# Performance work log

Hardware: AMD Instinct MI355X
Metric: run time of the kernel (lower is better)

Reference implementation:

```python
import jax, jax.numpy as jnp
import numpy as np

N = 20000          # nodes
F = 64             # num_features
H = 128            # hidden_channels
K = 6              # kNN neighbors (includes self, matching torch_cluster.knn(x, x, k))
E = 120000         # unused edge_index length


def knn_indices(x, k):
    # squared euclidean pairwise distances: [N, N]
    sq = jnp.sum(x * x, axis=-1)
    dist2 = sq[:, None] + sq[None, :] - 2.0 * (x @ x.T)
    # k smallest distances per row (self included, dist ~0)
    _, idx = jax.lax.top_k(-dist2, k)   # [N, K]
    return idx


def setup_inputs() -> dict:
    key = jax.random.key(0)
    ks = jax.random.split(key, 6)
    x = jax.random.normal(ks[0], (N, F), dtype=jnp.float32)
    edge_index = jax.random.randint(ks[1], (2, E), 0, N, dtype=jnp.int64)
    W1 = jax.random.normal(ks[2], (2 * F, H), dtype=jnp.float32) * 0.05
    b1 = jnp.zeros((H,), dtype=jnp.float32)
    W2 = jax.random.normal(ks[3], (H, H), dtype=jnp.float32) * 0.05
    b2 = jnp.zeros((H,), dtype=jnp.float32)
    return {"x": x, "edge_index": edge_index, "W1": W1, "b1": b1, "W2": W2, "b2": b2}


def reference(x, edge_index, W1, b1, W2, b2):
    # DynamicEdgeConv: recompute kNN graph each forward (edge_index arg unused, as in source)
    idx = knn_indices(x, K)                       # [N, K] neighbor indices j for each center i
    xi = jnp.broadcast_to(x[:, None, :], (N, K, F))  # center features
    xj = x[idx]                                   # neighbor features  [N, K, F]
    msg = jnp.concatenate([xi, xj - xi], axis=-1)    # [N, K, 2F]
    h = jax.nn.relu(jnp.einsum('nkf,fh->nkh', msg, W1) + b1)
    h = jnp.einsum('nkh,hg->nkg', h, W2) + b2     # [N, K, H]
    return jnp.max(h, axis=1)                     # max aggregation -> [N, H]
```

## Files before the change

kernel.cpp:

```cpp
#include <hip/hip_runtime.h>


#define N_NODES 20000
#define FDIM 64
#define KNN 6
#define HID 128
#define N_PAD 20480
#define NTILES 625
#define PREP_TILES 628
#define NBLK 157
#define NCHUNK 3
#define TPC 209
#define RPB 256
#define TILE_J 64
#define MAX_CHUNKS 10

typedef __attribute__((ext_vector_type(8))) short short8;
typedef __attribute__((ext_vector_type(16))) float f32x16;

#define MFMAB(A, B, C) __builtin_amdgcn_mfma_f32_32x32x16_bf16((A), (B), (C), 0, 0, 0)
#define ROFF(r) (((r) & 3) + 8 * ((r) >> 2))

#define INSERT_CAND(bd, bj, dv, jv) do {                                      \
  if ((dv) < bd[5]) {                                                         \
    const bool c0 = (dv) < bd[0], c1 = (dv) < bd[1], c2 = (dv) < bd[2];       \
    const bool c3 = (dv) < bd[3], c4 = (dv) < bd[4];                          \
    bd[5] = c4 ? bd[4] : (dv);              bj[5] = c4 ? bj[4] : (jv);        \
    bd[4] = c4 ? (c3 ? bd[3] : (dv)) : bd[4]; bj[4] = c4 ? (c3 ? bj[3] : (jv)) : bj[4]; \
    bd[3] = c3 ? (c2 ? bd[2] : (dv)) : bd[3]; bj[3] = c3 ? (c2 ? bj[2] : (jv)) : bj[3]; \
    bd[2] = c2 ? (c1 ? bd[1] : (dv)) : bd[2]; bj[2] = c2 ? (c1 ? bj[1] : (jv)) : bj[2]; \
    bd[1] = c1 ? (c0 ? bd[0] : (dv)) : bd[1]; bj[1] = c1 ? (c0 ? bj[0] : (jv)) : bj[1]; \
    bd[0] = c0 ? (dv) : bd[0];              bj[0] = c0 ? (jv) : bj[0];        \
  }                                                                           \
} while (0)

#define LEXLT(dv, jv, ds, js) (((dv) < (ds)) || ((dv) == (ds) && (jv) < (js)))
#define INSERT_TIE(bd, bj, dv, jv) do {                                       \
  if (LEXLT((dv), (jv), bd[5], bj[5])) {                                      \
    const bool c0 = LEXLT((dv), (jv), bd[0], bj[0]);                          \
    const bool c1 = LEXLT((dv), (jv), bd[1], bj[1]);                          \
    const bool c2 = LEXLT((dv), (jv), bd[2], bj[2]);                          \
    const bool c3 = LEXLT((dv), (jv), bd[3], bj[3]);                          \
    const bool c4 = LEXLT((dv), (jv), bd[4], bj[4]);                          \
    bd[5] = c4 ? bd[4] : (dv);              bj[5] = c4 ? bj[4] : (jv);        \
    bd[4] = c4 ? (c3 ? bd[3] : (dv)) : bd[4]; bj[4] = c4 ? (c3 ? bj[3] : (jv)) : bj[4]; \
    bd[3] = c3 ? (c2 ? bd[2] : (dv)) : bd[3]; bj[3] = c3 ? (c2 ? bj[2] : (jv)) : bj[3]; \
    bd[2] = c2 ? (c1 ? bd[1] : (dv)) : bd[2]; bj[2] = c2 ? (c1 ? bj[1] : (jv)) : bj[2]; \
    bd[1] = c1 ? (c0 ? bd[0] : (dv)) : bd[1]; bj[1] = c1 ? (c0 ? bj[0] : (jv)) : bj[1]; \
    bd[0] = c0 ? (dv) : bd[0];              bj[0] = c0 ? (jv) : bj[0];        \
  }                                                                           \
} while (0)

__device__ __forceinline__ f32x16 zero16() {
  f32x16 v;
#pragma unroll
  for (int i = 0; i < 16; ++i) v[i] = 0.f;
  return v;
}

__device__ __forceinline__ unsigned short bf16_rne(float x) {
  unsigned u = __float_as_uint(x);
  u += 0x7fffu + ((u >> 16) & 1u);
  return (unsigned short)(u >> 16);
}
__device__ __forceinline__ float bf16_tof(unsigned short h) {
  return __uint_as_float(((unsigned)h) << 16);
}

__global__ void prep_kernel(const float* __restrict__ x, short* __restrict__ xa,
                            short* __restrict__ xb, short* __restrict__ xc,
                            float* __restrict__ sq) {
  const int n = blockIdx.x * blockDim.x + threadIdx.x;
  if (n >= PREP_TILES * 32) return;
  const int tile = n >> 5, row = n & 31;
  unsigned short a[FDIM], b[FDIM], c[FDIM];
  float s = 0.f;
  if (n < N_NODES) {
    const float4* r4 = (const float4*)(x + (size_t)n * FDIM);
#pragma unroll
    for (int q = 0; q < 16; ++q) {
      const float4 v = r4[q];
      const float vv[4] = {v.x, v.y, v.z, v.w};
#pragma unroll
      for (int e = 0; e < 4; ++e) {
        const float xv = vv[e];
        s = fmaf(xv, xv, s);
        const unsigned short ua = bf16_rne(xv);
        const float r1 = xv - bf16_tof(ua);
        const unsigned short ub = bf16_rne(r1);
        const float r2 = r1 - bf16_tof(ub);
        a[q * 4 + e] = ua; b[q * 4 + e] = ub; c[q * 4 + e] = bf16_rne(r2);
      }
    }
  } else {
#pragma unroll
    for (int f = 0; f < FDIM; ++f) { a[f] = 0; b[f] = 0; c[f] = 0; }
    s = __builtin_inff();
  }
  sq[n] = s;
#pragma unroll
  for (int ks = 0; ks < 4; ++ks) {
#pragma unroll
    for (int hh = 0; hh < 2; ++hh) {
      short8 va, vb, vc;
#pragma unroll
      for (int j = 0; j < 8; ++j) {
        const int f = ks * 16 + hh * 8 + j;
        va[j] = (short)a[f]; vb[j] = (short)b[f]; vc[j] = (short)c[f];
      }
      const size_t off = (size_t)tile * 2048 + ks * 512 + (size_t)((hh << 5) | row) * 8;
      *(short8*)(xa + off) = va;
      *(short8*)(xb + off) = vb;
      *(short8*)(xc + off) = vc;
    }
  }
}

__device__ __forceinline__ void load_frag(const short* __restrict__ xa,
                                          const short* __restrict__ xb,
                                          const short* __restrict__ xc, int t,
                                          int lane, short8 (&Fa)[4],
                                          short8 (&Fb)[4], short8 (&Fc)[4]) {
  const size_t tb = (size_t)t * 2048 + (size_t)lane * 8;
#pragma unroll
  for (int ks = 0; ks < 4; ++ks) {
    Fa[ks] = *(const short8*)(xa + tb + ks * 512);
    Fb[ks] = *(const short8*)(xb + tb + ks * 512);
    Fc[ks] = *(const short8*)(xc + tb + ks * 512);
  }
}

__device__ __forceinline__ void select6(const f32x16& acc,
                                        const float (&sqa)[16], int jbase,
                                        float (&bd)[KNN], int (&bj)[KNN]) {
  float key[16];
#pragma unroll
  for (int r = 0; r < 16; ++r) key[r] = fmaf(-2.f, acc[r], sqa[r]);
  float m0 = key[0], m1 = __builtin_inff();
  int j0 = jbase + ROFF(0);
#pragma unroll
  for (int r = 1; r < 16; ++r) {
    const float kr = key[r];
    const bool lt = kr < m0;
    m1 = fminf(m1, lt ? m0 : kr);
    j0 = lt ? (jbase + ROFF(r)) : j0;
    m0 = lt ? kr : m0;
  }
  if (__any(m0 < bd[5])) {
    if (__any(m1 < bd[5])) {
#pragma unroll
      for (int r = 0; r < 16; ++r) { INSERT_CAND(bd, bj, key[r], jbase + ROFF(r)); }
    } else {
      INSERT_CAND(bd, bj, m0, j0);
    }
  }
}

__device__ __forceinline__ void xmerge(float (&bd)[KNN], int (&bj)[KNN]) {
  float od[KNN];
  int oj[KNN];
#pragma unroll
  for (int k = 0; k < KNN; ++k) {
    od[k] = __shfl_xor(bd[k], 32);
    oj[k] = __shfl_xor(bj[k], 32);
  }
#pragma unroll
  for (int k = 0; k < KNN; ++k) INSERT_TIE(bd, bj, od[k], oj[k]);
}

__global__ __launch_bounds__(256, 2) void knn_bf16_kernel(
    const short* __restrict__ xa, const short* __restrict__ xb,
    const short* __restrict__ xc, const float* __restrict__ sq,
    float* __restrict__ cand_d, unsigned short* __restrict__ cand_js,
    int* __restrict__ knn_idx, int nchunks) {
  __shared__ __align__(16) short sa[2048];
  __shared__ __align__(16) short sb[2048];
  __shared__ __align__(16) short sc[2048];
  const int tid = threadIdx.x;
  const int lane = tid & 63;
  const int w = tid >> 6;
  const int ct = blockIdx.x * 4 + w;
  const int jc = blockIdx.y;
  const int h = lane >> 5, col = lane & 31;

  short8 Ba[4], Bb[4], Bc[4];
  load_frag(xa, xb, xc, ct, lane, Ba, Bb, Bc);

  float bd[KNN];
  int bj[KNN];
#pragma unroll
  for (int k = 0; k < KNN; ++k) { bd[k] = __builtin_inff(); bj[k] = 0; }

  const int tbeg = jc * TPC;
  int tend = tbeg + TPC;
  if (tend > NTILES) tend = NTILES;

  const int t8 = tid * 8;
  for (int t = tbeg; t < tend; ++t) {
    const size_t tb = (size_t)t * 2048;
    __syncthreads();
    *(short8*)(sa + t8) = *(const short8*)(xa + tb + t8);
    *(short8*)(sb + t8) = *(const short8*)(xb + tb + t8);
    *(short8*)(sc + t8) = *(const short8*)(xc + tb + t8);
    __syncthreads();

    f32x16 acc = zero16();
    const int la8 = lane * 8;
#pragma unroll
    for (int ks = 0; ks < 4; ++ks) {
      const short8 Aa = *(const short8*)(sa + ks * 512 + la8);
      const short8 Ab = *(const short8*)(sb + ks * 512 + la8);
      const short8 Ac = *(const short8*)(sc + ks * 512 + la8);
      acc = MFMAB(Aa, Ba[ks], acc);
      acc = MFMAB(Aa, Bb[ks], acc);
      acc = MFMAB(Ab, Ba[ks], acc);
      acc = MFMAB(Aa, Bc[ks], acc);
      acc = MFMAB(Ac, Ba[ks], acc);
      acc = MFMAB(Ab, Bb[ks], acc);
    }
    const int sbase = t * 32 + 4 * h;
    float4 S4[4];
#pragma unroll
    for (int g = 0; g < 4; ++g) S4[g] = *(const float4*)(sq + sbase + 8 * g);
    const float sqa[16] = {S4[0].x, S4[0].y, S4[0].z, S4[0].w,
                           S4[1].x, S4[1].y, S4[1].z, S4[1].w,
                           S4[2].x, S4[2].y, S4[2].z, S4[2].w,
                           S4[3].x, S4[3].y, S4[3].z, S4[3].w};
    select6(acc, sqa, t * 32 + 4 * h, bd, bj);
  }

  xmerge(bd, bj);

  if (h == 0) {
    const int i = ct * 32 + col;
    if (i < N_NODES) {
      if (nchunks == 1) {
#pragma unroll
        for (int k = 0; k < KNN; ++k) knn_idx[(size_t)i * KNN + k] = bj[k];
      } else {
#pragma unroll
        for (int k = 0; k < KNN; ++k) {
          const size_t off = ((size_t)jc * KNN + k) * N_PAD + i;
          cand_d[off] = bd[k];
          cand_js[off] = (unsigned short)bj[k];
        }
      }
    }
  }
}

__global__ void knn_merge_u16_kernel(const float* __restrict__ cand_d,
                                     const unsigned short* __restrict__ cand_js,
                                     int* __restrict__ knn_idx, int nchunks) {
  const int i = blockIdx.x * blockDim.x + threadIdx.x;
  if (i >= N_NODES) return;
  float bd[KNN];
  int bj[KNN];
#pragma unroll
  for (int k = 0; k < KNN; ++k) { bd[k] = __builtin_inff(); bj[k] = 0; }
  for (int jc = 0; jc < nchunks; ++jc) {
#pragma unroll
    for (int k = 0; k < KNN; ++k) {
      const size_t off = ((size_t)jc * KNN + k) * N_PAD + i;
      const float d = cand_d[off];
      const int j = (int)cand_js[off];
      INSERT_CAND(bd, bj, d, j);
    }
  }
#pragma unroll
  for (int k = 0; k < KNN; ++k) knn_idx[(size_t)i * KNN + k] = bj[k];
}

__global__ void sq_kernel(const float* __restrict__ x, float* __restrict__ sq) {
  const int i = blockIdx.x * blockDim.x + threadIdx.x;
  if (i >= N_NODES) return;
  const float4* r4 = (const float4*)(x + (size_t)i * FDIM);
  float s = 0.f;
#pragma unroll
  for (int q = 0; q < 16; ++q) {
    const float4 a = r4[q];
    s = fmaf(a.x, a.x, s);
    s = fmaf(a.y, a.y, s);
    s = fmaf(a.z, a.z, s);
    s = fmaf(a.w, a.w, s);
  }
  sq[i] = s;
}

__global__ __launch_bounds__(RPB, 2) void knn_partial_kernel(
    const float* __restrict__ x, const float* __restrict__ sq,
    float* __restrict__ cand_d, int* __restrict__ cand_j,
    int* __restrict__ knn_idx, int jchunk, int nchunks) {
  __shared__ __align__(16) float xs[TILE_J][FDIM + 4];
  __shared__ float sqs[TILE_J];
  const int tid = threadIdx.x;
  const int i = blockIdx.x * RPB + tid;
  const bool valid = i < N_NODES;
  const int jc = blockIdx.y;

  float xi[FDIM];
  float sqi = 0.f;
  if (valid) {
    const float4* r4 = (const float4*)(x + (size_t)i * FDIM);
#pragma unroll
    for (int q = 0; q < 16; ++q) {
      const float4 a = r4[q];
      xi[q * 4 + 0] = a.x; xi[q * 4 + 1] = a.y;
      xi[q * 4 + 2] = a.z; xi[q * 4 + 3] = a.w;
    }
    sqi = sq[i];
  } else {
#pragma unroll
    for (int f = 0; f < FDIM; ++f) xi[f] = 0.f;
  }
#pragma unroll
  for (int f = 0; f < FDIM; ++f) asm volatile("" : "+v"(xi[f]));

  float bd[KNN];
  int bj[KNN];
#pragma unroll
  for (int k = 0; k < KNN; ++k) { bd[k] = __builtin_inff(); bj[k] = 0; }

  const int jcbase = jc * jchunk;
  for (int t0 = 0; t0 < jchunk; t0 += TILE_J) {
    const int jt = jcbase + t0;
    __syncthreads();
    {
      const int jj = tid >> 2;
      const int f0 = (tid & 3) * 16;
      const int j = jt + jj;
      float4* dst = (float4*)&xs[jj][f0];
      if (j < N_NODES) {
        const float4* src = (const float4*)(x + (size_t)j * FDIM + f0);
        dst[0] = src[0];
        dst[1] = src[1];
        dst[2] = src[2];
        dst[3] = src[3];
      } else {
        const float4 z = make_float4(0.f, 0.f, 0.f, 0.f);
        dst[0] = z; dst[1] = z; dst[2] = z; dst[3] = z;
      }
      if (tid < TILE_J) {
        const int j2 = jt + tid;
        sqs[tid] = (j2 < N_NODES) ? sq[j2] : 0.f;
      }
    }
    __syncthreads();
    const int rem = N_NODES - jt;
    const int jmax = rem < TILE_J ? rem : TILE_J;
    for (int jj = 0; jj < jmax; ++jj) {
      const float4* xr4 = (const float4*)&xs[jj][0];
      float dot = 0.f;
#pragma unroll
      for (int q = 0; q < 16; ++q) {
        const float4 v = xr4[q];
        dot = fmaf(xi[q * 4 + 0], v.x, dot);
        dot = fmaf(xi[q * 4 + 1], v.y, dot);
        dot = fmaf(xi[q * 4 + 2], v.z, dot);
        dot = fmaf(xi[q * 4 + 3], v.w, dot);
      }
      const float d = fmaf(-2.f, dot, sqi + sqs[jj]);
      const int j = jt + jj;
      INSERT_CAND(bd, bj, d, j);
    }
  }

  if (valid) {
    if (nchunks == 1) {
#pragma unroll
      for (int k = 0; k < KNN; ++k) knn_idx[(size_t)i * KNN + k] = bj[k];
    } else {
#pragma unroll
      for (int k = 0; k < KNN; ++k) {
        const size_t off = ((size_t)jc * KNN + k) * N_PAD + i;
        cand_d[off] = bd[k];
        cand_j[off] = bj[k];
      }
    }
  }
}

__global__ void knn_merge_kernel(const float* __restrict__ cand_d,
                                 const int* __restrict__ cand_j,
                                 int* __restrict__ knn_idx, int nchunks) {
  const int i = blockIdx.x * blockDim.x + threadIdx.x;
  if (i >= N_NODES) return;
  float bd[KNN];
  int bj[KNN];
#pragma unroll
  for (int k = 0; k < KNN; ++k) { bd[k] = __builtin_inff(); bj[k] = 0; }
  for (int jc = 0; jc < nchunks; ++jc) {
#pragma unroll
    for (int k = 0; k < KNN; ++k) {
      const size_t off = ((size_t)jc * KNN + k) * N_PAD + i;
      const float d = cand_d[off];
      const int j = cand_j[off];
      INSERT_CAND(bd, bj, d, j);
    }
  }
#pragma unroll
  for (int k = 0; k < KNN; ++k) knn_idx[(size_t)i * KNN + k] = bj[k];
}

__global__ __launch_bounds__(HID) void mlp_kernel(
    const float* __restrict__ x, const int* __restrict__ knn_idx,
    const float* __restrict__ W1, const float* __restrict__ b1,
    const float* __restrict__ W2, const float* __restrict__ b2,
    float* __restrict__ out) {
  __shared__ float xi_s[FDIM];
  __shared__ float xd_s[KNN][FDIM];
  __shared__ float h1_s[KNN][HID];
  __shared__ int nb[KNN];
  const int i = blockIdx.x;
  const int t = threadIdx.x;
  if (t < KNN) {
    const int v = knn_idx[(size_t)i * KNN + t];
    nb[t] = ((unsigned)v < (unsigned)N_NODES) ? v : 0;
  }
  if (t < FDIM) xi_s[t] = x[(size_t)i * FDIM + t];
  __syncthreads();
  for (int e = t; e < KNN * FDIM; e += HID) {
    const int k = e >> 6;
    const int f = e & 63;
    xd_s[k][f] = x[(size_t)nb[k] * FDIM + f] - xi_s[f];
  }
  __syncthreads();

  float s0 = b1[t];
  for (int f = 0; f < FDIM; ++f) {
    const float w = W1[f * HID + t];
    s0 = fmaf(xi_s[f], w, s0);
  }
  float acc[KNN];
#pragma unroll
  for (int k = 0; k < KNN; ++k) acc[k] = s0;
  for (int f = 0; f < FDIM; ++f) {
    const float w = W1[(FDIM + f) * HID + t];
#pragma unroll
    for (int k = 0; k < KNN; ++k) acc[k] = fmaf(xd_s[k][f], w, acc[k]);
  }
#pragma unroll
  for (int k = 0; k < KNN; ++k) h1_s[k][t] = fmaxf(acc[k], 0.f);
  __syncthreads();

  float acc2[KNN];
  const float bb = b2[t];
#pragma unroll
  for (int k = 0; k < KNN; ++k) acc2[k] = bb;
  for (int h = 0; h < HID; ++h) {
    const float w = W2[h * HID + t];
#pragma unroll
    for (int k = 0; k < KNN; ++k) acc2[k] = fmaf(h1_s[k][h], w, acc2[k]);
  }
  float m = acc2[0];
#pragma unroll
  for (int k = 1; k < KNN; ++k) m = fmaxf(m, acc2[k]);
  out[(size_t)i * HID + t] = m;
}

extern "C" void kernel_launch(void* const* d_in, const int* in_sizes, int n_in,
                              void* d_out, int out_size, void* d_ws, size_t ws_size,
                              hipStream_t stream) {
  const float* x  = (const float*)d_in[0];
  const float* W1 = (const float*)d_in[2];
  const float* b1 = (const float*)d_in[3];
  const float* W2 = (const float*)d_in[4];
  const float* b2 = (const float*)d_in[5];
  float* out = (float*)d_out;
  char* ws = (char*)d_ws;
  const size_t PER_CHUNK = (size_t)KNN * N_PAD * 8;

  if (ws_size >= 0x998000) {
    float* sq   = (float*)ws;
    short* xa   = (short*)(ws + 0x20000);
    short* xb   = (short*)(ws + 0x294000);
    short* xc   = (short*)(ws + 0x508000);
    float* cand_d = (float*)(ws + 0x77C000);
    unsigned short* cand_js = (unsigned short*)(ws + 0x8E4000);
    int* knn = (int*)(ws + 0x20000);

    prep_kernel<<<dim3((PREP_TILES * 32 + 255) / 256), dim3(256), 0, stream>>>(
        x, xa, xb, xc, sq);
    knn_bf16_kernel<<<dim3(NBLK, NCHUNK), dim3(256), 0, stream>>>(
        xa, xb, xc, sq, cand_d, cand_js, knn, NCHUNK);
    knn_merge_u16_kernel<<<dim3((N_NODES + 255) / 256), dim3(256), 0, stream>>>(
        cand_d, cand_js, knn, NCHUNK);
    mlp_kernel<<<dim3(N_NODES), dim3(HID), 0, stream>>>(x, knn, W1, b1, W2, b2, out);
  } else {
    float* sq = (float*)ws;
    int* knn  = (int*)(ws + (size_t)N_PAD * 4);
    const size_t BASE = 0x90000;
    int nc = 1;
    if (ws_size > BASE + PER_CHUNK) {
      size_t fit = (ws_size - BASE) / PER_CHUNK;
      nc = fit < (size_t)MAX_CHUNKS ? (int)fit : MAX_CHUNKS;
      if (nc < 1) nc = 1;
    }
    int jchunk = ((N_NODES + nc - 1) / nc + TILE_J - 1) / TILE_J * TILE_J;
    float* cand_d = (float*)(ws + BASE);
    int* cand_j = (int*)(ws + BASE + (size_t)nc * KNN * N_PAD * 4);

    sq_kernel<<<dim3((N_NODES + 255) / 256), dim3(256), 0, stream>>>(x, sq);
    knn_partial_kernel<<<dim3((N_NODES + RPB - 1) / RPB, nc), dim3(RPB), 0, stream>>>(
        x, sq, cand_d, cand_j, knn, jchunk, nc);
    if (nc > 1) {
      knn_merge_kernel<<<dim3((N_NODES + 255) / 256), dim3(256), 0, stream>>>(
          cand_d, cand_j, knn, nc);
    }
    mlp_kernel<<<dim3(N_NODES), dim3(HID), 0, stream>>>(x, knn, W1, b1, W2, b2, out);
  }
}
```

Measured before the change: 638.9 us.

## Double-buffer kNN tiles via direct global-to-LDS loads, two tiles per iteration

Replaces the register-staged LDS fill (two barriers per tile) with async global_load_lds into a double-buffered set holding two tiles. The next pair of tiles is prefetched while the current pair's MFMAs run. Two independent accumulator chains are interleaved to hide MFMA latency, and one barrier now covers two tiles. LDS use grows fourfold, to about 48KB per block, which may limit the targeted two blocks per CU. The code also relies on global_load_lds lane-address semantics and on the barrier waiting for the async loads to finish.

```diff
diff --git a/kernel.cpp b/kernel.cpp
--- a/kernel.cpp
+++ b/kernel.cpp
@@ -67,6 +67,12 @@
   return __uint_as_float(((unsigned)h) << 16);
 }
 
+__device__ __forceinline__ void gload_lds16(const void* g, void* l) {
+  __builtin_amdgcn_global_load_lds(
+      (const __attribute__((address_space(1))) void*)g,
+      (__attribute__((address_space(3))) void*)l, 16, 0, 0);
+}
+
 __global__ void prep_kernel(const float* __restrict__ x, short* __restrict__ xa,
                             short* __restrict__ xb, short* __restrict__ xc,
                             float* __restrict__ sq) {
@@ -156,6 +162,21 @@
   }
 }
 
+__device__ __forceinline__ void do_select(const f32x16& acc,
+                                          const float* __restrict__ sq, int t,
+                                          int h, float (&bd)[KNN],
+                                          int (&bj)[KNN]) {
+  const int sbase = t * 32 + 4 * h;
+  float4 S4[4];
+#pragma unroll
+  for (int g = 0; g < 4; ++g) S4[g] = *(const float4*)(sq + sbase + 8 * g);
+  const float sqa[16] = {S4[0].x, S4[0].y, S4[0].z, S4[0].w,
+                         S4[1].x, S4[1].y, S4[1].z, S4[1].w,
+                         S4[2].x, S4[2].y, S4[2].z, S4[2].w,
+                         S4[3].x, S4[3].y, S4[3].z, S4[3].w};
+  select6(acc, sqa, t * 32 + 4 * h, bd, bj);
+}
+
 __device__ __forceinline__ void xmerge(float (&bd)[KNN], int (&bj)[KNN]) {
   float od[KNN];
   int oj[KNN];
@@ -173,9 +194,9 @@
     const short* __restrict__ xc, const float* __restrict__ sq,
     float* __restrict__ cand_d, unsigned short* __restrict__ cand_js,
     int* __restrict__ knn_idx, int nchunks) {
-  __shared__ __align__(16) short sa[2048];
-  __shared__ __align__(16) short sb[2048];
-  __shared__ __align__(16) short sc[2048];
+  __shared__ __align__(16) short sa[2][2][2048];
+  __shared__ __align__(16) short sb[2][2][2048];
+  __shared__ __align__(16) short sc[2][2][2048];
   const int tid = threadIdx.x;
   const int lane = tid & 63;
   const int w = tid >> 6;
@@ -195,39 +216,58 @@
   int tend = tbeg + TPC;
   if (tend > NTILES) tend = NTILES;
 
-  const int t8 = tid * 8;
-  for (int t = tbeg; t < tend; ++t) {
-    const size_t tb = (size_t)t * 2048;
+  const int wo = w * 512;
+  const int go = wo + lane * 8;
+
+#define STAGE_PAIR_SLOT(set, slot, t)                                         \
+  do {                                                                        \
+    const size_t tb_ = (size_t)(t) * 2048 + go;                               \
+    gload_lds16(xa + tb_, &sa[set][slot][wo]);                                \
+    gload_lds16(xb + tb_, &sb[set][slot][wo]);                                \
+    gload_lds16(xc + tb_, &sc[set][slot][wo]);                                \
+  } while (0)
+
+  STAGE_PAIR_SLOT(0, 0, tbeg);
+  if (tbeg + 1 < tend) STAGE_PAIR_SLOT(0, 1, tbeg + 1);
+  __syncthreads();
+
+  int cur = 0;
+  for (int t = tbeg; t < tend; t += 2) {
+    const bool has2 = (t + 1 < tend);
+    if (t + 2 < tend) STAGE_PAIR_SLOT(cur ^ 1, 0, t + 2);
+    if (t + 3 < tend) STAGE_PAIR_SLOT(cur ^ 1, 1, t + 3);
+
+    f32x16 ac0 = zero16(), ac1 = zero16();
+    const int la8 = lane * 8;
+#pragma unroll
+    for (int ks = 0; ks < 4; ++ks) {
+      const int o = ks * 512 + la8;
+      const short8 A0a = *(const short8*)(&sa[cur][0][o]);
+      const short8 A0b = *(const short8*)(&sb[cur][0][o]);
+      const short8 A0c = *(const short8*)(&sc[cur][0][o]);
+      const short8 A1a = *(const short8*)(&sa[cur][1][o]);
+      const short8 A1b = *(const short8*)(&sb[cur][1][o]);
+      const short8 A1c = *(const short8*)(&sc[cur][1][o]);
+      ac0 = MFMAB(A0a, Ba[ks], ac0);
+      ac1 = MFMAB(A1a, Ba[ks], ac1);
+      ac0 = MFMAB(A0a, Bb[ks], ac0);
+      ac1 = MFMAB(A1a, Bb[ks], ac1);
+      ac0 = MFMAB(A0b, Ba[ks], ac0);
+      ac1 = MFMAB(A1b, Ba[ks], ac1);
+      ac0 = MFMAB(A0a, Bc[ks], ac0);
+      ac1 = MFMAB(A1a, Bc[ks], ac1);
+      ac0 = MFMAB(A0c, Ba[ks], ac0);
+      ac1 = MFMAB(A1c, Ba[ks], ac1);
+      ac0 = MFMAB(A0b, Bb[ks], ac0);
+      ac1 = MFMAB(A1b, Bb[ks], ac1);
+    }
+    do_select(ac0, sq, t, h, bd, bj);
+    if (has2) do_select(ac1, sq, t + 1, h, bd, bj);
+
     __syncthreads();
-    *(short8*)(sa + t8) = *(const short8*)(xa + tb + t8);
-    *(short8*)(sb + t8) = *(const short8*)(xb + tb + t8);
-    *(short8*)(sc + t8) = *(const short8*)(xc + tb + t8);
-    __syncthreads();
-
-    f32x16 acc = zero16();
-    const int la8 = lane * 8;
-#pragma unroll
-    for (int ks = 0; ks < 4; ++ks) {
-      const short8 Aa = *(const short8*)(sa + ks * 512 + la8);
-      const short8 Ab = *(const short8*)(sb + ks * 512 + la8);
-      const short8 Ac = *(const short8*)(sc + ks * 512 + la8);
-      acc = MFMAB(Aa, Ba[ks], acc);
-      acc = MFMAB(Aa, Bb[ks], acc);
-      acc = MFMAB(Ab, Ba[ks], acc);
-      acc = MFMAB(Aa, Bc[ks], acc);
-      acc = MFMAB(Ac, Ba[ks], acc);
-      acc = MFMAB(Ab, Bb[ks], acc);
-    }
-    const int sbase = t * 32 + 4 * h;
-    float4 S4[4];
-#pragma unroll
-    for (int g = 0; g < 4; ++g) S4[g] = *(const float4*)(sq + sbase + 8 * g);
-    const float sqa[16] = {S4[0].x, S4[0].y, S4[0].z, S4[0].w,
-                           S4[1].x, S4[1].y, S4[1].z, S4[1].w,
-                           S4[2].x, S4[2].y, S4[2].z, S4[2].w,
-                           S4[3].x, S4[3].y, S4[3].z, S4[3].w};
-    select6(acc, sqa, t * 32 + 4 * h, bd, bj);
-  }
+    cur ^= 1;
+  }
+#undef STAGE_PAIR_SLOT
 
   xmerge(bd, bj);
 
```

New measurement: 615.8 us. -3.6%, faster.

## Double-buffer kNN tiles with direct global-to-LDS loads and overlapped selection

Applied to the files above, without the earlier changes.

The kNN distance kernel now stages each 32-row tile into two LDS buffers using global_load_lds, which writes straight to shared memory without passing through registers. It interleaves the MFMA compute of one tile with the top-6 selection of the previous tile, so loads, matrix math and selection can overlap. The selection pre-filter becomes a tree min and drops the second-min fast path, so any hit now runs the full 16-candidate insert. This doubles LDS use, may lower occupancy, and adds prologue and epilogue handling for odd tile counts.

```diff
diff --git a/kernel.cpp b/kernel.cpp
--- a/kernel.cpp
+++ b/kernel.cpp
@@ -67,6 +67,12 @@
   return __uint_as_float(((unsigned)h) << 16);
 }
 
+__device__ __forceinline__ void gload_lds16(const void* g, void* l) {
+  __builtin_amdgcn_global_load_lds(
+      (const __attribute__((address_space(1))) void*)g,
+      (__attribute__((address_space(3))) void*)l, 16, 0, 0);
+}
+
 __global__ void prep_kernel(const float* __restrict__ x, short* __restrict__ xa,
                             short* __restrict__ xb, short* __restrict__ xc,
                             float* __restrict__ sq) {
@@ -130,29 +136,33 @@
   }
 }
 
-__device__ __forceinline__ void select6(const f32x16& acc,
-                                        const float (&sqa)[16], int jbase,
-                                        float (&bd)[KNN], int (&bj)[KNN]) {
+__device__ __forceinline__ void do_select(const f32x16& acc,
+                                          const float* __restrict__ sq, int t,
+                                          int h, float (&bd)[KNN],
+                                          int (&bj)[KNN]) {
+  const int sbase = t * 32 + 4 * h;
+  float4 S4[4];
+#pragma unroll
+  for (int g = 0; g < 4; ++g) S4[g] = *(const float4*)(sq + sbase + 8 * g);
+  const float sqa[16] = {S4[0].x, S4[0].y, S4[0].z, S4[0].w,
+                         S4[1].x, S4[1].y, S4[1].z, S4[1].w,
+                         S4[2].x, S4[2].y, S4[2].z, S4[2].w,
+                         S4[3].x, S4[3].y, S4[3].z, S4[3].w};
   float key[16];
 #pragma unroll
   for (int r = 0; r < 16; ++r) key[r] = fmaf(-2.f, acc[r], sqa[r]);
-  float m0 = key[0], m1 = __builtin_inff();
-  int j0 = jbase + ROFF(0);
-#pragma unroll
-  for (int r = 1; r < 16; ++r) {
-    const float kr = key[r];
-    const bool lt = kr < m0;
-    m1 = fminf(m1, lt ? m0 : kr);
-    j0 = lt ? (jbase + ROFF(r)) : j0;
-    m0 = lt ? kr : m0;
-  }
-  if (__any(m0 < bd[5])) {
-    if (__any(m1 < bd[5])) {
-#pragma unroll
-      for (int r = 0; r < 16; ++r) { INSERT_CAND(bd, bj, key[r], jbase + ROFF(r)); }
-    } else {
-      INSERT_CAND(bd, bj, m0, j0);
-    }
+  float m8[8];
+#pragma unroll
+  for (int r = 0; r < 8; ++r) m8[r] = fminf(key[r], key[r + 8]);
+  float m4[4];
+#pragma unroll
+  for (int r = 0; r < 4; ++r) m4[r] = fminf(m8[r], m8[r + 4]);
+  const float m2a = fminf(m4[0], m4[2]), m2b = fminf(m4[1], m4[3]);
+  const float m = fminf(m2a, m2b);
+  if (__any(m < bd[5])) {
+    const int jbase = t * 32 + 4 * h;
+#pragma unroll
+    for (int r = 0; r < 16; ++r) { INSERT_CAND(bd, bj, key[r], jbase + ROFF(r)); }
   }
 }
 
@@ -173,9 +183,9 @@
     const short* __restrict__ xc, const float* __restrict__ sq,
     float* __restrict__ cand_d, unsigned short* __restrict__ cand_js,
     int* __restrict__ knn_idx, int nchunks) {
-  __shared__ __align__(16) short sa[2048];
-  __shared__ __align__(16) short sb[2048];
-  __shared__ __align__(16) short sc[2048];
+  __shared__ __align__(16) short sa[2][2048];
+  __shared__ __align__(16) short sb[2][2048];
+  __shared__ __align__(16) short sc[2][2048];
   const int tid = threadIdx.x;
   const int lane = tid & 63;
   const int w = tid >> 6;
@@ -194,53 +204,78 @@
   const int tbeg = jc * TPC;
   int tend = tbeg + TPC;
   if (tend > NTILES) tend = NTILES;
-
-  const int t8 = tid * 8;
-  for (int t = tbeg; t < tend; ++t) {
-    const size_t tb = (size_t)t * 2048;
+  const int n = tend - tbeg;
+
+  const int wo = w * 512;
+  const int go = wo + lane * 8;
+  const int la8 = lane * 8;
+
+#define STAGE(set, t)                                                         \
+  do {                                                                        \
+    const size_t tb_ = (size_t)(t) * 2048 + go;                               \
+    gload_lds16(xa + tb_, &sa[set][wo]);                                      \
+    gload_lds16(xb + tb_, &sb[set][wo]);                                      \
+    gload_lds16(xc + tb_, &sc[set][wo]);                                      \
+  } while (0)
+
+#define COMPUTE_TILE(set, accvar)                                             \
+  do {                                                                        \
+    accvar = zero16();                                                        \
+    _Pragma("unroll")                                                         \
+    for (int ks = 0; ks < 4; ++ks) {                                          \
+      const int o_ = ks * 512 + la8;                                          \
+      const short8 Aa = *(const short8*)(&sa[set][o_]);                       \
+      const short8 Ab = *(const short8*)(&sb[set][o_]);                       \
+      const short8 Ac = *(const short8*)(&sc[set][o_]);                       \
+      accvar = MFMAB(Aa, Ba[ks], accvar);                                     \
+      accvar = MFMAB(Aa, Bb[ks], accvar);                                     \
+      accvar = MFMAB(Ab, Ba[ks], accvar);                                     \
+      accvar = MFMAB(Aa, Bc[ks], accvar);                                     \
+      accvar = MFMAB(Ac, Ba[ks], accvar);                                     \
+      accvar = MFMAB(Ab, Bb[ks], accvar);                                     \
+    }                                                                         \
+  } while (0)
+
+  STAGE(0, tbeg);
+  __syncthreads();
+  if (n > 1) STAGE(1, tbeg + 1);
+  f32x16 acA, acB;
+  COMPUTE_TILE(0, acA);
+  __syncthreads();
+
+  int i = 1;
+  for (; i + 1 < n; i += 2) {
+    STAGE(0, tbeg + i + 1);
+    COMPUTE_TILE(1, acB);
+    do_select(acA, sq, tbeg + i - 1, h, bd, bj);
     __syncthreads();
-    *(short8*)(sa + t8) = *(const short8*)(xa + tb + t8);
-    *(short8*)(sb + t8) = *(const short8*)(xb + tb + t8);
-    *(short8*)(sc + t8) = *(const short8*)(xc + tb + t8);
+    if (i + 2 < n) STAGE(1, tbeg + i + 2);
+    COMPUTE_TILE(0, acA);
+    do_select(acB, sq, tbeg + i, h, bd, bj);
     __syncthreads();
-
-    f32x16 acc = zero16();
-    const int la8 = lane * 8;
-#pragma unroll
-    for (int ks = 0; ks < 4; ++ks) {
-      const short8 Aa = *(const short8*)(sa + ks * 512 + la8);
-      const short8 Ab = *(const short8*)(sb + ks * 512 + la8);
-      const short8 Ac = *(const short8*)(sc + ks * 512 + la8);
-      acc = MFMAB(Aa, Ba[ks], acc);
-      acc = MFMAB(Aa, Bb[ks], acc);
-      acc = MFMAB(Ab, Ba[ks], acc);
-      acc = MFMAB(Aa, Bc[ks], acc);
-      acc = MFMAB(Ac, Ba[ks], acc);
-      acc = MFMAB(Ab, Bb[ks], acc);
-    }
-    const int sbase = t * 32 + 4 * h;
-    float4 S4[4];
-#pragma unroll
-    for (int g = 0; g < 4; ++g) S4[g] = *(const float4*)(sq + sbase + 8 * g);
-    const float sqa[16] = {S4[0].x, S4[0].y, S4[0].z, S4[0].w,
-                           S4[1].x, S4[1].y, S4[1].z, S4[1].w,
-                           S4[2].x, S4[2].y, S4[2].z, S4[2].w,
-                           S4[3].x, S4[3].y, S4[3].z, S4[3].w};
-    select6(acc, sqa, t * 32 + 4 * h, bd, bj);
-  }
+  }
+  if (i < n) {
+    COMPUTE_TILE(1, acB);
+    do_select(acA, sq, tbeg + i - 1, h, bd, bj);
+    do_select(acB, sq, tbeg + i, h, bd, bj);
+  } else {
+    do_select(acA, sq, tbeg + n - 1, h, bd, bj);
+  }
+#undef STAGE
+#undef COMPUTE_TILE
 
   xmerge(bd, bj);
 
   if (h == 0) {
-    const int i = ct * 32 + col;
-    if (i < N_NODES) {
+    const int i0 = ct * 32 + col;
+    if (i0 < N_NODES) {
       if (nchunks == 1) {
 #pragma unroll
-        for (int k = 0; k < KNN; ++k) knn_idx[(size_t)i * KNN + k] = bj[k];
+        for (int k = 0; k < KNN; ++k) knn_idx[(size_t)i0 * KNN + k] = bj[k];
       } else {
 #pragma unroll
         for (int k = 0; k < KNN; ++k) {
-          const size_t off = ((size_t)jc * KNN + k) * N_PAD + i;
+          const size_t off = ((size_t)jc * KNN + k) * N_PAD + i0;
           cand_d[off] = bd[k];
           cand_js[off] = (unsigned short)bj[k];
         }
```

Result: faster. 593.5 us (-7.1%).
